# Kernel optimization log

Hardware: AMD Instinct MI355X
Metric: run time of the kernel (lower is better)

## Reference

```python
import jax, jax.numpy as jnp
import numpy as np

N_NODES = 50000
N_EDGES = 800000
D_IN = 128
HIDDEN = 128
NUM_GRAPHS = 64
NUM_CLASSES = 6


def setup_inputs() -> dict:
    key = jax.random.key(0)
    ks = jax.random.split(key, 12)
    x = jax.random.normal(ks[0], (N_NODES, D_IN), dtype=jnp.float32)
    edge_index = jax.random.randint(ks[1], (2, N_EDGES), 0, N_NODES, dtype=jnp.int64)
    batch = jnp.sort(jax.random.randint(ks[2], (N_NODES,), 0, NUM_GRAPHS, dtype=jnp.int64))
    def glorot(k, fan_in, fan_out):
        s = jnp.sqrt(6.0 / (fan_in + fan_out)).astype(jnp.float32)
        return jax.random.uniform(k, (fan_in, fan_out), jnp.float32, -s, s)
    W0 = glorot(ks[3], D_IN, HIDDEN)
    b0 = jnp.zeros((HIDDEN,), jnp.float32)
    W1 = glorot(ks[4], HIDDEN, HIDDEN)
    b1 = jnp.zeros((HIDDEN,), jnp.float32)
    W2 = glorot(ks[5], HIDDEN, HIDDEN)
    b2 = jnp.zeros((HIDDEN,), jnp.float32)
    lin_W = glorot(ks[6], HIDDEN, NUM_CLASSES)
    lin_b = jnp.zeros((NUM_CLASSES,), jnp.float32)
    return {"x": x, "edge_index": edge_index, "batch": batch,
            "W0": W0, "b0": b0, "W1": W1, "b1": b1, "W2": W2, "b2": b2,
            "lin_W": lin_W, "lin_b": lin_b}


def reference(x, edge_index, batch, W0, b0, W1, b1, W2, b2, lin_W, lin_b):
    # GCNConv (PyG default): add self-loops, symmetric degree norm,
    # out = scatter_add(norm * (xW)[src] -> dst) + bias, then ReLU.
    loop = jnp.arange(N_NODES, dtype=edge_index.dtype)
    src = jnp.concatenate([edge_index[0], loop])  # message sources (x_j)
    dst = jnp.concatenate([edge_index[1], loop])  # aggregation targets
    deg = jax.ops.segment_sum(jnp.ones_like(dst, x.dtype), dst, num_segments=N_NODES)
    dinv = jnp.where(deg > 0, jax.lax.rsqrt(deg), 0.0)
    norm = (dinv[src] * dinv[dst])[:, None]  # [E+N, 1]

    h = x
    for W, b in ((W0, b0), (W1, b1), (W2, b2)):
        hw = h @ W                                   # [N, H] dense projection
        agg = jax.ops.segment_sum(hw[src] * norm, dst, num_segments=N_NODES)
        h = jax.nn.relu(agg + b)

    # global_mean_pool over graph ids
    counts = jax.ops.segment_sum(jnp.ones((N_NODES,), x.dtype), batch, num_segments=NUM_GRAPHS)
    embedding = jax.ops.segment_sum(h, batch, num_segments=NUM_GRAPHS) / jnp.maximum(counts, 1.0)[:, None]
    # dropout is identity in eval mode
    logits = embedding @ lin_W + lin_b
    return logits, embedding
```

## Files before the change

kernel.cpp:

```cpp
#include <hip/hip_runtime.h>

#define N_NODES 50000
#define HIDDEN 128
#define NUM_GRAPHS 64
#define NUM_CLASSES 6
#define SLOT_SHIFT 6
#define NB 782
#define NPAD 50048
#define ZROW 50040
#define BUCKET_CAP 1536
#define P1_CHUNK 2048
#define CONV_BLOCKS 96
#define LSTR 136

typedef __attribute__((ext_vector_type(8))) short short8;
typedef __attribute__((ext_vector_type(4))) float float4v;
typedef __attribute__((ext_vector_type(2))) float float2v;

__device__ __forceinline__ unsigned short f2b(float f) {
    unsigned u = __float_as_uint(f);
    return (unsigned short)((u + 0x7FFFu + ((u >> 16) & 1u)) >> 16);
}
__device__ __forceinline__ unsigned char f2e4m3(float f) {
    return (unsigned char)(__builtin_amdgcn_cvt_pk_fp8_f32(f, f, 0, false) & 0xFF);
}

__global__ __launch_bounds__(512) void pass1(const float* __restrict__ W0, const float* __restrict__ W1,
                                             const float* __restrict__ W2, unsigned short* __restrict__ wb,
                                             const int* __restrict__ src, const int* __restrict__ dst,
                                             int* __restrict__ gcursor, unsigned* __restrict__ ebuf, int e) {
    if (blockIdx.x < CONV_BLOCKS) {
        int i = blockIdx.x * 512 + threadIdx.x;
        int wsel = i >> 14;
        int r = i & 16383;
        int j = r & 7;
        int lane = (r >> 3) & 63;
        int f = r >> 9;
        int ki = f >> 3, nt = f & 7;
        int k = ki * 32 + (lane >> 4) * 8 + j;
        int c = nt * 16 + (lane & 15);
        const float* W = (wsel == 0) ? W0 : ((wsel == 1) ? W1 : W2);
        wb[i] = f2b(W[k * 128 + c]);
        return;
    }
    __shared__ unsigned hist[NB];
    __shared__ unsigned base[NB];
    const int t = threadIdx.x;
    const int start = (blockIdx.x - CONV_BLOCKS) * P1_CHUNK;
    for (int i = t; i < NB; i += 512) hist[i] = 0;
    __syncthreads();
    int lb[4];
    unsigned pk[4], lr[4];
#pragma unroll
    for (int k = 0; k < 4; k++) {
        int i = start + k * 512 + t;
        lb[k] = -1;
        if (i < e) {
            int d = dst[i];
            int s = src[i];
            lb[k] = d >> 6;
            pk[k] = ((unsigned)(d & 63) << 16) | (unsigned)s;
            lr[k] = atomicAdd(&hist[lb[k]], 1u);
        }
    }
    __syncthreads();
    for (int b = t; b < NB; b += 512)
        base[b] = (unsigned)atomicAdd(&gcursor[b], (int)hist[b]);
    __syncthreads();
#pragma unroll
    for (int k = 0; k < 4; k++) {
        if (lb[k] >= 0) {
            unsigned pos = base[lb[k]] + lr[k];
            if (pos < BUCKET_CAP) ebuf[lb[k] * BUCKET_CAP + pos] = pk[k];
        }
    }
}

__global__ __launch_bounds__(512) void pass2(const unsigned* __restrict__ ebuf, const int* __restrict__ gcursor,
                                             const float* __restrict__ x,
                                             unsigned short* __restrict__ csr16, int* __restrict__ cntc,
                                             float* __restrict__ dinv, unsigned char* __restrict__ xs8,
                                             unsigned char* __restrict__ h8a, unsigned char* __restrict__ h8b,
                                             int n) {
    __shared__ unsigned short csr_lds[64 * 64];
    __shared__ unsigned cnt[64];
    const int b = blockIdx.x;
    const int t = threadIdx.x;
    {
        const unsigned zz = ((unsigned)ZROW) | (((unsigned)ZROW) << 16);
        unsigned* cl = (unsigned*)csr_lds;
#pragma unroll
        for (int it = 0; it < 4; it++) cl[it * 512 + t] = zz;
    }
    if (t < 64) cnt[t] = 0;
    __syncthreads();
    if (t < 64) csr_lds[t * 64] = (unsigned short)(b * 64 + t);
    __syncthreads();
    const int nb = min(gcursor[b], BUCKET_CAP);
    for (int i = t; i < nb; i += 512) {
        unsigned e = ebuf[b * BUCKET_CAP + i];
        int dl = (int)(e >> 16);
        unsigned r = atomicAdd(&cnt[dl], 1u);
        if (r < 63) csr_lds[dl * 64 + 1 + r] = (unsigned short)(e & 0xFFFFu);
    }
    __syncthreads();
    {
        const unsigned* cu = (const unsigned*)csr_lds;
        unsigned* gout = (unsigned*)(csr16 + (size_t)b * 4096);
#pragma unroll
        for (int it = 0; it < 4; it++) gout[it * 512 + t] = cu[it * 512 + t];
    }
    if (t < 64) {
        int node = b * 64 + t;
        if (node < n) {
            int deg1 = (int)cnt[t] + 1;
            cntc[node] = min(deg1, 64);
            dinv[node] = rsqrtf((float)deg1);
        }
    }
#pragma unroll
    for (int it = 0; it < 4; it++) {
        int idx = it * 512 + t;
        int nl = idx >> 5;
        int el = (idx & 31) * 4;
        int gnode = b * 64 + nl;
        if (gnode < n) {
            float sc = rsqrtf((float)((int)cnt[nl] + 1));
            float4 v = *(const float4*)&x[gnode * 128 + el];
            unsigned lo = __builtin_amdgcn_cvt_pk_fp8_f32(v.x * sc, v.y * sc, 0, false);
            unsigned pkd = __builtin_amdgcn_cvt_pk_fp8_f32(v.z * sc, v.w * sc, lo, true);
            *(unsigned*)&xs8[gnode * 128 + el] = pkd;
        }
    }
    if (b == 0 && t < 384) {
        uint4 z = {0, 0, 0, 0};
        ((uint4*)(xs8 + (size_t)N_NODES * 128))[t] = z;
        ((uint4*)(h8a + (size_t)N_NODES * 128))[t] = z;
        ((uint4*)(h8b + (size_t)N_NODES * 128))[t] = z;
    }
}

template <bool LAST>
__global__ __launch_bounds__(256) void fused_layer(const unsigned char* __restrict__ hs8,
                                                   const int* __restrict__ cntc,
                                                   const unsigned short* __restrict__ csr16,
                                                   const float* __restrict__ dinv,
                                                   const unsigned short* __restrict__ wb,
                                                   const float* __restrict__ bias,
                                                   unsigned char* __restrict__ hout8,
                                                   const int* __restrict__ batchp,
                                                   float* __restrict__ embp) {
    __shared__ __align__(16) unsigned short tlds[16 * LSTR];
    __shared__ int bsh[16];
    const int wave = threadIdx.x >> 6;
    const int lane = threadIdx.x & 63;
    const int grp = lane >> 4;
    const int fl = lane & 15;
    const int node0 = blockIdx.x * 16;
    const int base_node = node0 + wave * 4;

    int nbv[4], mycv[4];
#pragma unroll
    for (int i = 0; i < 4; i++) nbv[i] = cntc[base_node + i];
#pragma unroll
    for (int i = 0; i < 4; i++)
        mycv[i] = (int)csr16[((base_node + i) << SLOT_SHIFT) + lane];

    for (int i = 0; i < 4; i++) {
        const int node = base_node + i;
        const int ng = (nbv[i] + 15) >> 4;
        const int myc = mycv[i];
        float2v a01 = {0.f, 0.f}, a23 = {0.f, 0.f}, a45 = {0.f, 0.f}, a67 = {0.f, 0.f};

        for (int g4 = 0; g4 < ng; g4++) {
            const int base = g4 << 4;
            int cc[4];
#pragma unroll
            for (int k = 0; k < 4; k++) cc[k] = __shfl(myc, base + k * 4 + grp, 64);
            uint2 u[4];
#pragma unroll
            for (int k = 0; k < 4; k++) u[k] = *(const uint2*)&hs8[cc[k] * 128 + fl * 8];
#pragma unroll
            for (int k = 0; k < 4; k++) {
                a01 += __builtin_amdgcn_cvt_pk_f32_fp8(u[k].x, false);
                a23 += __builtin_amdgcn_cvt_pk_f32_fp8(u[k].x, true);
                a45 += __builtin_amdgcn_cvt_pk_f32_fp8(u[k].y, false);
                a67 += __builtin_amdgcn_cvt_pk_f32_fp8(u[k].y, true);
            }
        }

        float acc[8] = {a01.x, a01.y, a23.x, a23.y, a45.x, a45.y, a67.x, a67.y};
#pragma unroll
        for (int j = 0; j < 8; j++) {
            acc[j] += __shfl_xor(acc[j], 16, 64);
            acc[j] += __shfl_xor(acc[j], 32, 64);
        }
        if (grp == 0) {
            const float dv = dinv[node];
            short8 o;
#pragma unroll
            for (int j = 0; j < 8; j++) o[j] = (short)f2b(acc[j] * dv);
            *(short8*)&tlds[(wave * 4 + i) * LSTR + fl * 8] = o;
        }
    }
    if (LAST && threadIdx.x < 16) bsh[threadIdx.x] = batchp[node0 + threadIdx.x];
    __syncthreads();

    const int m = fl;
    const int quad = grp;
    const int nt0 = wave * 2;
    const short* B = (const short*)wb;
    float4v acc2[2];
    acc2[0] = (float4v){0.f, 0.f, 0.f, 0.f};
    acc2[1] = (float4v){0.f, 0.f, 0.f, 0.f};
#pragma unroll
    for (int ki = 0; ki < 4; ki++) {
        short8 a = *(const short8*)&tlds[m * LSTR + ki * 32 + quad * 8];
#pragma unroll
        for (int q = 0; q < 2; q++) {
            short8 b = *(const short8*)&B[((ki * 8 + nt0 + q) * 64 + lane) * 8];
            acc2[q] = __builtin_amdgcn_mfma_f32_16x16x32_bf16(a, b, acc2[q], 0, 0, 0);
        }
    }

    if (!LAST) {
        float sc[4];
#pragma unroll
        for (int reg = 0; reg < 4; reg++) sc[reg] = dinv[node0 + quad * 4 + reg];
#pragma unroll
        for (int q = 0; q < 2; q++) {
            int c = (nt0 + q) * 16 + m;
            float bv = bias[c];
#pragma unroll
            for (int reg = 0; reg < 4; reg++) {
                int row = node0 + quad * 4 + reg;
                float v = fmaxf(acc2[q][reg] + bv, 0.f) * sc[reg];
                hout8[row * 128 + c] = f2e4m3(v);
            }
        }
    } else {
        const int g0 = bsh[0], g15 = bsh[15];
#pragma unroll
        for (int q = 0; q < 2; q++) {
            int c = (nt0 + q) * 16 + m;
            float bv = bias[c];
            float v0 = fmaxf(acc2[q][0] + bv, 0.f);
            float v1 = fmaxf(acc2[q][1] + bv, 0.f);
            float v2 = fmaxf(acc2[q][2] + bv, 0.f);
            float v3 = fmaxf(acc2[q][3] + bv, 0.f);
            if (g0 == g15) {
                float s = v0 + v1 + v2 + v3;
                s += __shfl_xor(s, 16, 64);
                s += __shfl_xor(s, 32, 64);
                if (quad == 0) atomicAdd(&embp[g0 * HIDDEN + c], s);
            } else {
                for (int gg = g0; gg <= g15; ++gg) {
                    float s = (bsh[quad * 4 + 0] == gg ? v0 : 0.f)
                            + (bsh[quad * 4 + 1] == gg ? v1 : 0.f)
                            + (bsh[quad * 4 + 2] == gg ? v2 : 0.f)
                            + (bsh[quad * 4 + 3] == gg ? v3 : 0.f);
                    s += __shfl_xor(s, 16, 64);
                    s += __shfl_xor(s, 32, 64);
                    if (quad == 0) atomicAdd(&embp[gg * HIDDEN + c], s);
                }
            }
        }
    }
}

__global__ __launch_bounds__(128) void finalize_kernel(const float* __restrict__ emb,
                                                       const int* __restrict__ batch,
                                                       const float* __restrict__ linW, const float* __restrict__ linb,
                                                       float* out, int n) {
    const int g = blockIdx.x;
    const int f = threadIdx.x;
    __shared__ float es[128];
    __shared__ int bnd[2];
    if (f < 2) {
        int target = g + f;
        int lo = 0, hi = n;
        while (lo < hi) {
            int mid = (lo + hi) >> 1;
            if (batch[mid] < target) lo = mid + 1; else hi = mid;
        }
        bnd[f] = lo;
    }
    __syncthreads();
    float c = (float)max(bnd[1] - bnd[0], 1);
    float e = emb[g * HIDDEN + f] / c;
    out[NUM_GRAPHS * NUM_CLASSES + g * HIDDEN + f] = e;
    es[f] = e;
    __syncthreads();
    if (f < NUM_CLASSES) {
        float s = linb[f];
        for (int k = 0; k < HIDDEN; k++) s += es[k] * linW[k * NUM_CLASSES + f];
        out[g * NUM_CLASSES + f] = s;
    }
}

extern "C" void kernel_launch(void* const* d_in, const int* in_sizes, int n_in,
                              void* d_out, int out_size, void* d_ws, size_t ws_size,
                              hipStream_t stream) {
    const float* x    = (const float*)d_in[0];
    const int*   ei   = (const int*)d_in[1];
    const int*   batch= (const int*)d_in[2];
    const float* W0   = (const float*)d_in[3];
    const float* b0   = (const float*)d_in[4];
    const float* W1   = (const float*)d_in[5];
    const float* b1   = (const float*)d_in[6];
    const float* W2   = (const float*)d_in[7];
    const float* b2   = (const float*)d_in[8];
    const float* linW = (const float*)d_in[9];
    const float* linb = (const float*)d_in[10];
    float* out = (float*)d_out;

    const int N = N_NODES;
    const int E = in_sizes[1] / 2;
    const int* srcp = ei;
    const int* dstp = ei + E;

    char* w = (char*)d_ws;
    size_t o = 0;
    auto alloc = [&](size_t bytes) { size_t r = o; o += (bytes + 255) & ~(size_t)255; return r; };
    int*            gcursor = (int*)           (w + alloc((size_t)NB * 4));
    float*          emb     = (float*)         (w + alloc((size_t)NUM_GRAPHS * HIDDEN * 4));
    size_t zero_bytes = o;
    unsigned*       ebuf    = (unsigned*)      (w + alloc((size_t)NB * BUCKET_CAP * 4));
    unsigned short* csr16   = (unsigned short*)(w + alloc((size_t)NB * 64 * 64 * 2));
    int*            cntc    = (int*)           (w + alloc((size_t)N * 4));
    float*          dinv    = (float*)         (w + alloc((size_t)N * 4));
    unsigned char*  xs8     = (unsigned char*) (w + alloc((size_t)NPAD * HIDDEN));
    unsigned char*  h8a     = (unsigned char*) (w + alloc((size_t)NPAD * HIDDEN));
    unsigned char*  h8b     = (unsigned char*) (w + alloc((size_t)NPAD * HIDDEN));
    unsigned short* wb      = (unsigned short*)(w + alloc((size_t)3 * 16384 * 2));

    hipMemsetAsync(d_ws, 0, zero_bytes, stream);

    const int p1_edge_blocks = (E + P1_CHUNK - 1) / P1_CHUNK;

    pass1<<<CONV_BLOCKS + p1_edge_blocks, 512, 0, stream>>>(W0, W1, W2, wb, srcp, dstp, gcursor, ebuf, E);
    pass2<<<NB, 512, 0, stream>>>(ebuf, gcursor, x, csr16, cntc, dinv, xs8, h8a, h8b, N);

    const int fuse_grid = N / 16;

    fused_layer<false><<<fuse_grid, 256, 0, stream>>>(xs8, cntc, csr16, dinv, wb + 0 * 16384, b0, h8a,
                                                      nullptr, nullptr);
    fused_layer<false><<<fuse_grid, 256, 0, stream>>>(h8a, cntc, csr16, dinv, wb + 1 * 16384, b1, h8b,
                                                      nullptr, nullptr);
    fused_layer<true><<<fuse_grid, 256, 0, stream>>>(h8b, cntc, csr16, dinv, wb + 2 * 16384, b2, nullptr,
                                                     batch, emb);

    finalize_kernel<<<NUM_GRAPHS, 128, 0, stream>>>(emb, batch, linW, linb, out, N);
}
```

Baseline: 196.9 us.

## Interleave gather of two nodes per wave and trim padded neighbor groups

The aggregation loop now processes two destination nodes at once, issuing the fp8 row loads for both before accumulating, so more independent memory requests are in flight per wave. Neighbor lists are walked in full 16-edge groups and then in 4-edge quads, instead of rounding up to 16 and gathering padding rows. The bucket-cursor atomic in pass1 is also skipped when a block's local histogram count is zero. The cost is higher register pressure and more code paths for uneven neighbor counts.

```diff
diff --git a/kernel.cpp b/kernel.cpp
--- a/kernel.cpp
+++ b/kernel.cpp
@@ -23,6 +23,12 @@
 }
 __device__ __forceinline__ unsigned char f2e4m3(float f) {
     return (unsigned char)(__builtin_amdgcn_cvt_pk_fp8_f32(f, f, 0, false) & 0xFF);
+}
+__device__ __forceinline__ void acc8(float2v (&A)[4], uint2 u) {
+    A[0] += __builtin_amdgcn_cvt_pk_f32_fp8(u.x, false);
+    A[1] += __builtin_amdgcn_cvt_pk_f32_fp8(u.x, true);
+    A[2] += __builtin_amdgcn_cvt_pk_f32_fp8(u.y, false);
+    A[3] += __builtin_amdgcn_cvt_pk_f32_fp8(u.y, true);
 }
 
 __global__ __launch_bounds__(512) void pass1(const float* __restrict__ W0, const float* __restrict__ W1,
@@ -64,8 +70,10 @@
         }
     }
     __syncthreads();
-    for (int b = t; b < NB; b += 512)
-        base[b] = (unsigned)atomicAdd(&gcursor[b], (int)hist[b]);
+    for (int b = t; b < NB; b += 512) {
+        unsigned h = hist[b];
+        base[b] = h ? (unsigned)atomicAdd(&gcursor[b], (int)h) : 0u;
+    }
     __syncthreads();
 #pragma unroll
     for (int k = 0; k < 4; k++) {
@@ -166,41 +174,103 @@
     for (int i = 0; i < 4; i++)
         mycv[i] = (int)csr16[((base_node + i) << SLOT_SHIFT) + lane];
 
-    for (int i = 0; i < 4; i++) {
-        const int node = base_node + i;
-        const int ng = (nbv[i] + 15) >> 4;
-        const int myc = mycv[i];
-        float2v a01 = {0.f, 0.f}, a23 = {0.f, 0.f}, a45 = {0.f, 0.f}, a67 = {0.f, 0.f};
-
-        for (int g4 = 0; g4 < ng; g4++) {
-            const int base = g4 << 4;
-            int cc[4];
-#pragma unroll
-            for (int k = 0; k < 4; k++) cc[k] = __shfl(myc, base + k * 4 + grp, 64);
-            uint2 u[4];
-#pragma unroll
-            for (int k = 0; k < 4; k++) u[k] = *(const uint2*)&hs8[cc[k] * 128 + fl * 8];
-#pragma unroll
-            for (int k = 0; k < 4; k++) {
-                a01 += __builtin_amdgcn_cvt_pk_f32_fp8(u[k].x, false);
-                a23 += __builtin_amdgcn_cvt_pk_f32_fp8(u[k].x, true);
-                a45 += __builtin_amdgcn_cvt_pk_f32_fp8(u[k].y, false);
-                a67 += __builtin_amdgcn_cvt_pk_f32_fp8(u[k].y, true);
-            }
-        }
-
-        float acc[8] = {a01.x, a01.y, a23.x, a23.y, a45.x, a45.y, a67.x, a67.y};
+#pragma unroll
+    for (int p = 0; p < 2; p++) {
+        const int iA = p * 2, iB = p * 2 + 1;
+        const int nbA = nbv[iA], nbB = nbv[iB];
+        const int mycA = mycv[iA], mycB = mycv[iB];
+        float2v aA[4], aB[4];
+#pragma unroll
+        for (int k = 0; k < 4; k++) { aA[k] = (float2v){0.f, 0.f}; aB[k] = (float2v){0.f, 0.f}; }
+
+        const int fA = nbA >> 4, fB = nbB >> 4;
+        const int c16 = min(fA, fB);
+        for (int g = 0; g < c16; g++) {
+            const int base = g << 4;
+            int cA[4], cB[4];
+#pragma unroll
+            for (int k = 0; k < 4; k++) cA[k] = __shfl(mycA, base + k * 4 + grp, 64);
+#pragma unroll
+            for (int k = 0; k < 4; k++) cB[k] = __shfl(mycB, base + k * 4 + grp, 64);
+            uint2 uA[4], uB[4];
+#pragma unroll
+            for (int k = 0; k < 4; k++) uA[k] = *(const uint2*)&hs8[cA[k] * 128 + fl * 8];
+#pragma unroll
+            for (int k = 0; k < 4; k++) uB[k] = *(const uint2*)&hs8[cB[k] * 128 + fl * 8];
+#pragma unroll
+            for (int k = 0; k < 4; k++) acc8(aA, uA[k]);
+#pragma unroll
+            for (int k = 0; k < 4; k++) acc8(aB, uB[k]);
+        }
+        for (int g = c16; g < fA; g++) {
+            const int base = g << 4;
+            int cA[4];
+#pragma unroll
+            for (int k = 0; k < 4; k++) cA[k] = __shfl(mycA, base + k * 4 + grp, 64);
+            uint2 uA[4];
+#pragma unroll
+            for (int k = 0; k < 4; k++) uA[k] = *(const uint2*)&hs8[cA[k] * 128 + fl * 8];
+#pragma unroll
+            for (int k = 0; k < 4; k++) acc8(aA, uA[k]);
+        }
+        for (int g = c16; g < fB; g++) {
+            const int base = g << 4;
+            int cB[4];
+#pragma unroll
+            for (int k = 0; k < 4; k++) cB[k] = __shfl(mycB, base + k * 4 + grp, 64);
+            uint2 uB[4];
+#pragma unroll
+            for (int k = 0; k < 4; k++) uB[k] = *(const uint2*)&hs8[cB[k] * 128 + fl * 8];
+#pragma unroll
+            for (int k = 0; k < 4; k++) acc8(aB, uB[k]);
+        }
+        const int nqA = (nbA + 3) >> 2, nqB = (nbB + 3) >> 2;
+        const int qA0 = fA << 2, qB0 = fB << 2;
+        const int ct = min(nqA - qA0, nqB - qB0);
+        for (int q = 0; q < ct; q++) {
+            int cA = __shfl(mycA, ((qA0 + q) << 2) + grp, 64);
+            int cB = __shfl(mycB, ((qB0 + q) << 2) + grp, 64);
+            uint2 uA = *(const uint2*)&hs8[cA * 128 + fl * 8];
+            uint2 uB = *(const uint2*)&hs8[cB * 128 + fl * 8];
+            acc8(aA, uA);
+            acc8(aB, uB);
+        }
+        for (int q = qA0 + ct; q < nqA; q++) {
+            int cA = __shfl(mycA, (q << 2) + grp, 64);
+            uint2 uA = *(const uint2*)&hs8[cA * 128 + fl * 8];
+            acc8(aA, uA);
+        }
+        for (int q = qB0 + ct; q < nqB; q++) {
+            int cB = __shfl(mycB, (q << 2) + grp, 64);
+            uint2 uB = *(const uint2*)&hs8[cB * 128 + fl * 8];
+            acc8(aB, uB);
+        }
+
+        float accR[8] = {aA[0].x, aA[0].y, aA[1].x, aA[1].y, aA[2].x, aA[2].y, aA[3].x, aA[3].y};
 #pragma unroll
         for (int j = 0; j < 8; j++) {
-            acc[j] += __shfl_xor(acc[j], 16, 64);
-            acc[j] += __shfl_xor(acc[j], 32, 64);
+            accR[j] += __shfl_xor(accR[j], 16, 64);
+            accR[j] += __shfl_xor(accR[j], 32, 64);
         }
         if (grp == 0) {
-            const float dv = dinv[node];
+            const float dv = dinv[base_node + iA];
             short8 o;
 #pragma unroll
-            for (int j = 0; j < 8; j++) o[j] = (short)f2b(acc[j] * dv);
-            *(short8*)&tlds[(wave * 4 + i) * LSTR + fl * 8] = o;
+            for (int j = 0; j < 8; j++) o[j] = (short)f2b(accR[j] * dv);
+            *(short8*)&tlds[(wave * 4 + iA) * LSTR + fl * 8] = o;
+        }
+        float accS[8] = {aB[0].x, aB[0].y, aB[1].x, aB[1].y, aB[2].x, aB[2].y, aB[3].x, aB[3].y};
+#pragma unroll
+        for (int j = 0; j < 8; j++) {
+            accS[j] += __shfl_xor(accS[j], 16, 64);
+            accS[j] += __shfl_xor(accS[j], 32, 64);
+        }
+        if (grp == 0) {
+            const float dv = dinv[base_node + iB];
+            short8 o;
+#pragma unroll
+            for (int j = 0; j < 8; j++) o[j] = (short)f2b(accS[j] * dv);
+            *(short8*)&tlds[(wave * 4 + iB) * LSTR + fl * 8] = o;
         }
     }
     if (LAST && threadIdx.x < 16) bsh[threadIdx.x] = batchp[node0 + threadIdx.x];
```

New measurement: 215.2 us. 9.3% more time.
